# Kernel optimization log

Hardware: AMD Instinct MI355X
Metric: run time of the kernel (lower is better)

Reference implementation:

```python
import jax, jax.numpy as jnp
import numpy as np

B, N, K = 4, 2048, 48
NUM_RBF = 16
NUM_PE = 16
MAX_REL = 32
EDGE_C = 128
PE_IN = 2 * MAX_REL + 2  # 66


def setup_inputs() -> dict:
    key = jax.random.key(0)
    ks = jax.random.split(key, 10)
    coords = jax.random.normal(ks[0], (B, N, 3), dtype=jnp.float32) * 10.0
    token_exists_mask = jnp.ones((B, N), dtype=jnp.float32)
    token_bonds = (jax.random.uniform(ks[1], (B, N, N)) < 0.01).astype(jnp.float32)
    pe_w = jax.random.normal(ks[2], (PE_IN, NUM_PE), dtype=jnp.float32) * 0.05
    pe_b = jnp.zeros((NUM_PE,), dtype=jnp.float32)
    edge_w = jax.random.normal(ks[3], (NUM_PE + NUM_RBF + 1, EDGE_C), dtype=jnp.float32) * 0.05
    ln_g = jnp.ones((EDGE_C,), dtype=jnp.float32)
    ln_b = jnp.zeros((EDGE_C,), dtype=jnp.float32)
    token_to_center_atom = jax.random.randint(ks[4], (B, N), 0, N, dtype=jnp.int32)
    residue_index = jnp.sort(jax.random.randint(ks[5], (B, N), 0, 4096, dtype=jnp.int32), axis=-1)
    asym_id = jax.random.randint(ks[6], (B, N), 0, 4, dtype=jnp.int32)
    is_ligand = jax.random.randint(ks[7], (B, N), 0, 2, dtype=jnp.int32)
    return {
        'coords': coords, 'token_exists_mask': token_exists_mask,
        'token_bonds': token_bonds, 'pe_w': pe_w, 'pe_b': pe_b,
        'edge_w': edge_w, 'ln_g': ln_g, 'ln_b': ln_b,
        'token_to_center_atom': token_to_center_atom,
        'residue_index': residue_index, 'asym_id': asym_id,
        'is_ligand': is_ligand,
    }


def _gather_edges(M, E_idx):
    # M: [B, N, N], E_idx: [B, N, K] -> [B, N, K]
    return jnp.take_along_axis(M, E_idx, axis=2)


def _rbf(D):
    # D: [..., K] -> [..., K, NUM_RBF]
    D_mu = jnp.linspace(2.0, 22.0, NUM_RBF)
    D_sigma = (22.0 - 2.0) / NUM_RBF
    return jnp.exp(-(((D[..., None] - D_mu) / D_sigma) ** 2))


def reference(coords, token_exists_mask, token_bonds, pe_w, pe_b, edge_w,
              ln_g, ln_b, token_to_center_atom, residue_index, asym_id, is_ligand):
    # token coords: center atom per token, masked
    X = jnp.take_along_axis(coords, token_to_center_atom[..., None], axis=1)
    X = X * token_exists_mask[..., None]  # [B, N, 3]

    # masked pairwise distances + KNN (smallest K, sorted ascending)
    mask = token_exists_mask
    mask_2d = mask[:, None, :] * mask[:, :, None]  # [B, N, N]
    dX = X[:, :, None, :] - X[:, None, :, :]
    D = mask_2d * jnp.sqrt(jnp.sum(dX * dX, axis=-1) + 1e-6)
    D_max = jnp.max(D, axis=-1, keepdims=True)
    D_adjust = D + (1.0 - mask_2d) * D_max
    neg_D, E_idx = jax.lax.top_k(-D_adjust, K)  # largest of -D == smallest of D
    D_neighbors = -neg_D  # [B, N, K]

    RBF_all = _rbf(D_neighbors)  # [B, N, K, NUM_RBF]

    # relative sequence position features
    offset = residue_index[:, :, None] - residue_index[:, None, :]  # [B, N, N]
    offset_e = _gather_edges(offset, E_idx)  # [B, N, K]
    chain_labels = jnp.zeros_like(asym_id)  # use_multichain_encoding=False
    d_chains = (chain_labels[:, :, None] - chain_labels[:, None, :] == 0).astype(jnp.int32)
    E_chains = _gather_edges(d_chains, E_idx)  # [B, N, K]
    d = jnp.clip(offset_e + MAX_REL, 0, 2 * MAX_REL) * E_chains + (1 - E_chains) * (2 * MAX_REL + 1)
    d_onehot = jax.nn.one_hot(d, PE_IN, dtype=jnp.float32)
    E_positional = d_onehot @ pe_w + pe_b  # [B, N, K, NUM_PE]

    # ligand-gated bond feature
    lig = is_ligand.astype(bool)
    tb_mask = (lig[:, :, None] | lig[:, None, :]).astype(token_bonds.dtype)
    tb = token_bonds * tb_mask
    tb_e = _gather_edges(tb, E_idx)[..., None]  # [B, N, K, 1]

    # fuse, embed, layernorm
    E = jnp.concatenate([E_positional, RBF_all, tb_e], axis=-1)  # [B, N, K, 33]
    E = E @ edge_w  # [B, N, K, EDGE_C]
    mu = jnp.mean(E, axis=-1, keepdims=True)
    var = jnp.mean((E - mu) ** 2, axis=-1, keepdims=True)
    E = (E - mu) / jnp.sqrt(var + 1e-5) * ln_g + ln_b
    return (E, E_idx, D_neighbors)
```

## Files before the change

### kernel.cpp

```cpp
#include <hip/hip_runtime.h>
#include <math.h>

namespace {
constexpr int B_ = 4;
constexpr int N_ = 2048;
constexpr int K_ = 48;
constexpr int MAX_REL_ = 32;
constexpr int EDGE_C_ = 128;
constexpr int NUM_PE_ = 16;
constexpr int NROWS = B_ * N_;
constexpr int NEDGE = NROWS * K_;
constexpr int C1_ROWS = 2 * MAX_REL_ + 1;
}

__global__ __launch_bounds__(256) void x_kernel(const float* __restrict__ coords,
                                                const float* __restrict__ mask,
                                                const int* __restrict__ t2ca,
                                                float* __restrict__ X) {
    int r = blockIdx.x * 256 + threadIdx.x;
    if (r >= NROWS) return;
    int b = r >> 11;
    int c = t2ca[r];
    float m = mask[r];
    const float* s = coords + ((size_t)(b * N_ + c)) * 3;
    X[r * 3 + 0] = __fmul_rn(s[0], m);
    X[r * 3 + 1] = __fmul_rn(s[1], m);
    X[r * 3 + 2] = __fmul_rn(s[2], m);
}

__global__ __launch_bounds__(256) void c1_kernel(const float* __restrict__ pe_w,
                                                 const float* __restrict__ pe_b,
                                                 const float* __restrict__ edge_w,
                                                 float* __restrict__ C1) {
    int idx = blockIdx.x * 256 + threadIdx.x;
    if (idx >= C1_ROWS * EDGE_C_) return;
    int d = idx >> 7, c = idx & 127;
    float acc = 0.0f;
    #pragma unroll
    for (int p = 0; p < NUM_PE_; ++p)
        acc = fmaf(pe_w[d * NUM_PE_ + p] + pe_b[p], edge_w[p * EDGE_C_ + c], acc);
    C1[idx] = acc;
}

__global__ __launch_bounds__(128) void knn_kernel(const float* __restrict__ X,
                                                  const float* __restrict__ mask,
                                                  float* __restrict__ eidx_f,
                                                  float* __restrict__ dneb) {
    __shared__ unsigned long long skey[2][32][64];
    const int wv = threadIdx.x >> 6;
    const int lane = threadIdx.x & 63;
    const int row = blockIdx.x * 2 + wv;
    const int b = row >> 11;

    const float xi0 = X[row * 3 + 0];
    const float xi1 = X[row * 3 + 1];
    const float xi2 = X[row * 3 + 2];
    const float mi = mask[row];
    const float* Xb = X + (size_t)b * N_ * 3;
    const float* mb = mask + b * N_;

    float d[32];
    float lmax = -INFINITY;
    #pragma unroll
    for (int t = 0; t < 32; ++t) {
        int j = t * 64 + lane;
        float dx = __fsub_rn(xi0, Xb[j * 3 + 0]);
        float dy = __fsub_rn(xi1, Xb[j * 3 + 1]);
        float dz = __fsub_rn(xi2, Xb[j * 3 + 2]);
        float d2 = __fmaf_rn(dz, dz, __fmaf_rn(dx, dx, __fmul_rn(dy, dy)));
        float m2 = __fmul_rn(mi, mb[j]);
        float dd = __fmul_rn(m2, __fsqrt_rn(__fadd_rn(d2, 1e-6f)));
        d[t] = dd;
        lmax = fmaxf(lmax, dd);
    }
    #pragma unroll
    for (int off = 32; off; off >>= 1) lmax = fmaxf(lmax, __shfl_xor(lmax, off, 64));

    unsigned long long key[32];
    #pragma unroll
    for (int t = 0; t < 32; ++t) {
        int j = t * 64 + lane;
        float m2 = __fmul_rn(mi, mb[j]);
        float adj = __fadd_rn(d[t], __fmul_rn(__fsub_rn(1.0f, m2), lmax));
        key[t] = ((unsigned long long)__float_as_uint(adj) << 11) | (unsigned long long)j;
    }

    #pragma unroll
    for (int kk = 2; kk <= 32; kk <<= 1) {
        #pragma unroll
        for (int jj = kk >> 1; jj > 0; jj >>= 1) {
            #pragma unroll
            for (int i = 0; i < 32; ++i) {
                int l = i ^ jj;
                if (l > i) {
                    const bool dir = ((i & kk) == 0);
                    unsigned long long a = key[i], b2 = key[l];
                    unsigned long long lo = a < b2 ? a : b2;
                    unsigned long long hi = a < b2 ? b2 : a;
                    key[i] = dir ? lo : hi;
                    key[l] = dir ? hi : lo;
                }
            }
        }
    }

    #pragma unroll
    for (int t = 0; t < 32; ++t) skey[wv][t][lane] = key[t];
    __syncthreads();

    unsigned long long hd = key[0];
    unsigned long long nxt = key[1];
    int ptr = 2;

    unsigned long long res = 0;
    for (int k = 0; k < K_; ++k) {
        unsigned long long v = hd;
        #pragma unroll
        for (int off = 32; off; off >>= 1) {
            unsigned long long o = __shfl_xor(v, off, 64);
            v = (o < v) ? o : v;
        }
        if (hd == v) {
            hd = nxt;
            unsigned long long t = skey[wv][ptr & 31][lane];
            nxt = (ptr < 32) ? t : ~0ull;
            ++ptr;
        }
        if (lane == k) res = v;
    }

    if (lane < K_) {
        unsigned int fb = (unsigned int)(res >> 11);
        unsigned int ji = (unsigned int)(res & 2047u);
        dneb[(size_t)row * K_ + lane] = __uint_as_float(fb);
        eidx_f[(size_t)row * K_ + lane] = (float)ji;
    }
}

__global__ __launch_bounds__(256, 4) void edge_kernel(const float* __restrict__ eidx_f,
                                                      const float* __restrict__ dneb,
                                                      const float* __restrict__ token_bonds,
                                                      const float* __restrict__ C1,
                                                      const float* __restrict__ edge_w,
                                                      const float* __restrict__ ln_g,
                                                      const float* __restrict__ ln_b,
                                                      const int* __restrict__ res_idx,
                                                      const int* __restrict__ is_lig,
                                                      float* __restrict__ Eout) {
    __shared__ float s_rbf[4][K_][NUM_PE_];
    __shared__ float s_D[4][K_];
    const int tid = threadIdx.x;
    const int wv = tid >> 6;
    const int lane = tid & 63;
    const int row = blockIdx.x * 4 + wv;
    const int b = row >> 11;

    float w0[17], w1[17];
    #pragma unroll
    for (int p = 0; p < 17; ++p) {
        float2 w = ((const float2*)edge_w)[(NUM_PE_ + p) * 64 + lane];
        w0[p] = w.x; w1[p] = w.y;
    }
    const float g0 = ln_g[2 * lane], g1 = ln_g[2 * lane + 1];
    const float bb0 = ln_b[2 * lane], bb1 = ln_b[2 * lane + 1];

    const int ri = res_idx[row];
    const int li = is_lig[row];

    int doff_l = 0; float tb_l = 0.0f;
    if (lane < K_) {
        const int e = row * K_ + lane;
        const int j = (int)(eidx_f[e] + 0.5f);
        const float D = dneb[e];
        const int jrow = b * N_ + j;
        const int rj = res_idx[jrow];
        const int lj = is_lig[jrow];
        float tb = token_bonds[(size_t)row * N_ + j];
        tb_l = (li | lj) ? tb : 0.0f;
        doff_l = min(max(ri - rj + MAX_REL_, 0), 2 * MAX_REL_);
        s_D[wv][lane] = D;
    }
    __syncthreads();

    #pragma unroll
    for (int t = 0; t < (K_ * NUM_PE_) / 64; ++t) {
        const int idx = t * 64 + lane;
        const int k = idx >> 4, r = idx & 15;
        const float D = s_D[wv][k];
        const float mu = 2.0f + (float)r * (4.0f / 3.0f);
        const float x = (D - mu) * 0.8f;
        s_rbf[wv][k][r] = __expf(-x * x);
    }
    __syncthreads();

    float2* outp = (float2*)Eout + (size_t)row * K_ * 64 + lane;
    #pragma unroll 2
    for (int k = 0; k < K_; ++k) {
        const int doffk = __shfl(doff_l, k, 64);
        const float tbk = __shfl(tb_l, k, 64);
        const float2 c1 = *(const float2*)(C1 + ((size_t)doffk << 7) + 2 * lane);

        float rr[16];
        *(float4*)&rr[0]  = *(const float4*)&s_rbf[wv][k][0];
        *(float4*)&rr[4]  = *(const float4*)&s_rbf[wv][k][4];
        *(float4*)&rr[8]  = *(const float4*)&s_rbf[wv][k][8];
        *(float4*)&rr[12] = *(const float4*)&s_rbf[wv][k][12];

        float ax = 0.0f, ay = 0.0f;
        #pragma unroll
        for (int p = 0; p < 16; ++p) {
            ax = fmaf(rr[p], w0[p], ax);
            ay = fmaf(rr[p], w1[p], ay);
        }
        if (tbk != 0.0f) {
            ax = fmaf(tbk, w0[16], ax);
            ay = fmaf(tbk, w1[16], ay);
        }
        ax += c1.x; ay += c1.y;

        float s = ax + ay, sq = fmaf(ax, ax, ay * ay);
        #pragma unroll
        for (int off = 32; off; off >>= 1) {
            s  += __shfl_xor(s, off, 64);
            sq += __shfl_xor(sq, off, 64);
        }
        const float mu = s * (1.0f / 128.0f);
        const float var = sq * (1.0f / 128.0f) - mu * mu;
        const float rstd = rsqrtf(var + 1e-5f);
        const float ox = (ax - mu) * rstd * g0 + bb0;
        const float oy = (ay - mu) * rstd * g1 + bb1;
        outp[(size_t)k * 64] = make_float2(ox, oy);
    }
}

extern "C" void kernel_launch(void* const* d_in, const int* in_sizes, int n_in,
                              void* d_out, int out_size, void* d_ws, size_t ws_size,
                              hipStream_t stream) {
    const float* coords      = (const float*)d_in[0];
    const float* mask        = (const float*)d_in[1];
    const float* token_bonds = (const float*)d_in[2];
    const float* pe_w        = (const float*)d_in[3];
    const float* pe_b        = (const float*)d_in[4];
    const float* edge_w      = (const float*)d_in[5];
    const float* ln_g        = (const float*)d_in[6];
    const float* ln_b        = (const float*)d_in[7];
    const int*   t2ca        = (const int*)d_in[8];
    const int*   res_idx     = (const int*)d_in[9];
    const int*   is_lig      = (const int*)d_in[11];

    float* out    = (float*)d_out;
    float* Eout   = out;
    float* eidx_f = out + (size_t)NEDGE * EDGE_C_;
    float* dneb   = eidx_f + NEDGE;

    float* X  = (float*)d_ws;
    float* C1 = X + (size_t)NROWS * 3;

    hipLaunchKernelGGL(x_kernel, dim3(NROWS / 256), dim3(256), 0, stream,
                       coords, mask, t2ca, X);
    hipLaunchKernelGGL(c1_kernel, dim3((C1_ROWS * EDGE_C_ + 255) / 256), dim3(256), 0, stream,
                       pe_w, pe_b, edge_w, C1);
    hipLaunchKernelGGL(knn_kernel, dim3(NROWS / 2), dim3(128), 0, stream,
                       X, mask, eidx_f, dneb);
    hipLaunchKernelGGL(edge_kernel, dim3(NROWS / 4), dim3(256), 0, stream,
                       eidx_f, dneb, token_bonds, C1, edge_w,
                       ln_g, ln_b, res_idx, is_lig, Eout);
}
```

Measured before the change: 443.6 us.

## Replace per-lane bitonic sort with radix-select top-K in KNN kernel

The KNN kernel previously bitonic-sorted 32 64-bit keys per lane in registers and then ran a 48-step wave-wide merge. It now rebases the distance bits to the row minimum and does an MSB-first 8-bit radix select with per-wave shared-memory histograms to find the K-th key threshold. It then compacts the keys at or below the threshold and bitonic-sorts those 48 across the wave with shuffles. Blocks now hold 4 waves instead of 2. This removes a large register sort but adds LDS atomics and a data-dependent number of histogram passes, and relies on the keys being unique.

```diff
diff --git a/kernel.cpp b/kernel.cpp
--- a/kernel.cpp
+++ b/kernel.cpp
@@ -42,14 +42,15 @@
     C1[idx] = acc;
 }
 
-__global__ __launch_bounds__(128) void knn_kernel(const float* __restrict__ X,
+__global__ __launch_bounds__(256) void knn_kernel(const float* __restrict__ X,
                                                   const float* __restrict__ mask,
                                                   float* __restrict__ eidx_f,
                                                   float* __restrict__ dneb) {
-    __shared__ unsigned long long skey[2][32][64];
+    __shared__ unsigned s_hist[4][256];
+    __shared__ unsigned long long s_cbuf[4][64];
     const int wv = threadIdx.x >> 6;
     const int lane = threadIdx.x & 63;
-    const int row = blockIdx.x * 2 + wv;
+    const int row = blockIdx.x * 4 + wv;
     const int b = row >> 11;
 
     const float xi0 = X[row * 3 + 0];
@@ -76,63 +77,136 @@
     #pragma unroll
     for (int off = 32; off; off >>= 1) lmax = fmaxf(lmax, __shfl_xor(lmax, off, 64));
 
-    unsigned long long key[32];
+    unsigned fb[32];
+    unsigned fmin_l = 0xFFFFFFFFu, fmax_l = 0u;
     #pragma unroll
     for (int t = 0; t < 32; ++t) {
         int j = t * 64 + lane;
         float m2 = __fmul_rn(mi, mb[j]);
         float adj = __fadd_rn(d[t], __fmul_rn(__fsub_rn(1.0f, m2), lmax));
-        key[t] = ((unsigned long long)__float_as_uint(adj) << 11) | (unsigned long long)j;
-    }
-
-    #pragma unroll
-    for (int kk = 2; kk <= 32; kk <<= 1) {
-        #pragma unroll
-        for (int jj = kk >> 1; jj > 0; jj >>= 1) {
-            #pragma unroll
-            for (int i = 0; i < 32; ++i) {
-                int l = i ^ jj;
-                if (l > i) {
-                    const bool dir = ((i & kk) == 0);
-                    unsigned long long a = key[i], b2 = key[l];
-                    unsigned long long lo = a < b2 ? a : b2;
-                    unsigned long long hi = a < b2 ? b2 : a;
-                    key[i] = dir ? lo : hi;
-                    key[l] = dir ? hi : lo;
-                }
+        unsigned u = __float_as_uint(adj);
+        fb[t] = u;
+        fmin_l = min(fmin_l, u);
+        fmax_l = max(fmax_l, u);
+    }
+    #pragma unroll
+    for (int off = 32; off; off >>= 1) {
+        fmin_l = min(fmin_l, (unsigned)__shfl_xor((int)fmin_l, off, 64));
+        fmax_l = max(fmax_l, (unsigned)__shfl_xor((int)fmax_l, off, 64));
+    }
+    const unsigned fminb = fmin_l;
+    const unsigned range = fmax_l - fminb;
+    const int vbits = (range == 0u) ? 0 : (32 - __clz((int)range));
+    const int L = vbits + 11;
+
+    unsigned long long key[32];
+    #pragma unroll
+    for (int t = 0; t < 32; ++t)
+        key[t] = ((unsigned long long)(fb[t] - fminb) << 11)
+               | (unsigned long long)(unsigned)(t * 64 + lane);
+
+    unsigned cand = 0xFFFFFFFFu;
+    int k_rem = K_;
+    int sh = (L > 8) ? (L - 8) : 0;
+    unsigned long long T = 0ull;
+
+    while (true) {
+        s_hist[wv][4 * lane + 0] = 0u;
+        s_hist[wv][4 * lane + 1] = 0u;
+        s_hist[wv][4 * lane + 2] = 0u;
+        s_hist[wv][4 * lane + 3] = 0u;
+        __asm__ volatile("s_waitcnt lgkmcnt(0)" ::: "memory");
+        #pragma unroll
+        for (int t = 0; t < 32; ++t) {
+            if ((cand >> t) & 1u) {
+                unsigned dig = (unsigned)(key[t] >> sh) & 255u;
+                atomicAdd(&s_hist[wv][dig], 1u);
             }
         }
-    }
-
-    #pragma unroll
-    for (int t = 0; t < 32; ++t) skey[wv][t][lane] = key[t];
-    __syncthreads();
-
-    unsigned long long hd = key[0];
-    unsigned long long nxt = key[1];
-    int ptr = 2;
-
-    unsigned long long res = 0;
-    for (int k = 0; k < K_; ++k) {
-        unsigned long long v = hd;
-        #pragma unroll
-        for (int off = 32; off; off >>= 1) {
-            unsigned long long o = __shfl_xor(v, off, 64);
-            v = (o < v) ? o : v;
-        }
-        if (hd == v) {
-            hd = nxt;
-            unsigned long long t = skey[wv][ptr & 31][lane];
-            nxt = (ptr < 32) ? t : ~0ull;
-            ++ptr;
-        }
-        if (lane == k) res = v;
+        __asm__ volatile("s_waitcnt lgkmcnt(0)" ::: "memory");
+        const unsigned c0 = s_hist[wv][4 * lane + 0];
+        const unsigned c1 = s_hist[wv][4 * lane + 1];
+        const unsigned c2 = s_hist[wv][4 * lane + 2];
+        const unsigned c3 = s_hist[wv][4 * lane + 3];
+        const unsigned s4 = c0 + c1 + c2 + c3;
+        unsigned inc = s4;
+        #pragma unroll
+        for (int off = 1; off < 64; off <<= 1) {
+            unsigned o = (unsigned)__shfl_up((int)inc, off, 64);
+            if (lane >= off) inc += o;
+        }
+        const unsigned ex = inc - s4;
+        const unsigned e1 = ex + c0, e2 = e1 + c1, e3 = e2 + c2;
+        const unsigned kr = (unsigned)k_rem;
+        int digl = -1; unsigned below = 0u, bc = 0u;
+        if (ex < kr && kr <= e1)           { digl = 4 * lane + 0; below = ex; bc = c0; }
+        else if (e1 < kr && kr <= e2)      { digl = 4 * lane + 1; below = e1; bc = c1; }
+        else if (e2 < kr && kr <= e3)      { digl = 4 * lane + 2; below = e2; bc = c2; }
+        else if (e3 < kr && kr <= e3 + c3) { digl = 4 * lane + 3; below = e3; bc = c3; }
+
+        unsigned long long bal = __ballot(digl >= 0);
+        int src = __ffsll((long long)bal) - 1;
+        const int dstar = __shfl(digl, src, 64);
+        below = (unsigned)__shfl((int)below, src, 64);
+        bc    = (unsigned)__shfl((int)bc, src, 64);
+        k_rem -= (int)below;
+
+        unsigned nc = 0u;
+        unsigned long long myT = 0ull;
+        #pragma unroll
+        for (int t = 0; t < 32; ++t) {
+            if (((cand >> t) & 1u) &&
+                (((unsigned)(key[t] >> sh) & 255u) == (unsigned)dstar)) {
+                nc |= (1u << t);
+                myT = key[t];
+            }
+        }
+        cand = nc;
+        if (bc == 1u || sh == 0) {
+            unsigned long long b2 = __ballot(cand != 0u);
+            int owner = __ffsll((long long)b2) - 1;
+            T = __shfl(myT, owner, 64);
+            break;
+        }
+        sh = (sh > 8) ? (sh - 8) : 0;
+    }
+
+    unsigned selm = 0u; int scnt = 0;
+    #pragma unroll
+    for (int t = 0; t < 32; ++t) {
+        if (key[t] <= T) { selm |= (1u << t); ++scnt; }
+    }
+    int isc = scnt;
+    #pragma unroll
+    for (int off = 1; off < 64; off <<= 1) {
+        int o = __shfl_up(isc, off, 64);
+        if (lane >= off) isc += o;
+    }
+    int pos = isc - scnt;
+    #pragma unroll
+    for (int t = 0; t < 32; ++t) {
+        if ((selm >> t) & 1u) { s_cbuf[wv][pos] = key[t]; ++pos; }
+    }
+    __asm__ volatile("s_waitcnt lgkmcnt(0)" ::: "memory");
+    unsigned long long kk = (lane < K_) ? s_cbuf[wv][lane] : ~0ull;
+
+    #pragma unroll
+    for (int k2 = 2; k2 <= 64; k2 <<= 1) {
+        #pragma unroll
+        for (int j = k2 >> 1; j > 0; j >>= 1) {
+            unsigned long long o = __shfl_xor(kk, j, 64);
+            const bool dirAsc = ((lane & k2) == 0);
+            const bool lower = ((lane & j) == 0);
+            unsigned long long mn = (kk < o) ? kk : o;
+            unsigned long long mx = (kk < o) ? o : kk;
+            kk = (lower == dirAsc) ? mn : mx;
+        }
     }
 
     if (lane < K_) {
-        unsigned int fb = (unsigned int)(res >> 11);
-        unsigned int ji = (unsigned int)(res & 2047u);
-        dneb[(size_t)row * K_ + lane] = __uint_as_float(fb);
+        unsigned fbits = (unsigned)(kk >> 11) + fminb;
+        unsigned ji = (unsigned)(kk & 2047u);
+        dneb[(size_t)row * K_ + lane] = __uint_as_float(fbits);
         eidx_f[(size_t)row * K_ + lane] = (float)ji;
     }
 }
@@ -260,7 +334,7 @@
                        coords, mask, t2ca, X);
     hipLaunchKernelGGL(c1_kernel, dim3((C1_ROWS * EDGE_C_ + 255) / 256), dim3(256), 0, stream,
                        pe_w, pe_b, edge_w, C1);
-    hipLaunchKernelGGL(knn_kernel, dim3(NROWS / 2), dim3(128), 0, stream,
+    hipLaunchKernelGGL(knn_kernel, dim3(NROWS / 4), dim3(256), 0, stream,
                        X, mask, eidx_f, dneb);
     hipLaunchKernelGGL(edge_kernel, dim3(NROWS / 4), dim3(256), 0, stream,
                        eidx_f, dneb, token_bonds, C1, edge_w,
```

Result: faster. 382.1 us (-13.9%).
